# Kernel tuning notes

Hardware: AMD Instinct MI355X
Metric: run time of the kernel (lower is better)

Reference implementation:

```python
import jax, jax.numpy as jnp
import numpy as np

B, T, NN, H = 16, 64, 4096, 1024  # batch, seq_len, num_nodes**2, gru hidden


def _gru_layer(x, w_ih, w_hh, b_ih, b_hh):
    """PyTorch-semantics GRU layer, batch_first. x: [B, T, in] -> [B, T, H]."""
    h_dim = w_hh.shape[1]
    # precompute all input-side gate projections in one GEMM: [B, T, 3H]
    gates_x = jnp.einsum('bti,gi->btg', x, w_ih) + b_ih

    def step(h, gx):
        gh = h @ w_hh.T + b_hh                      # [B, 3H]
        xr, xz, xn = jnp.split(gx, 3, axis=-1)
        hr, hz, hn = jnp.split(gh, 3, axis=-1)
        r = jax.nn.sigmoid(xr + hr)
        z = jax.nn.sigmoid(xz + hz)
        n = jnp.tanh(xn + r * hn)
        h_new = (1.0 - z) * n + z * h
        return h_new, h_new

    h0 = jnp.zeros((x.shape[0], h_dim), x.dtype)
    _, ys = jax.lax.scan(step, h0, jnp.swapaxes(gates_x, 0, 1))  # time-major scan
    return jnp.swapaxes(ys, 0, 1)


def setup_inputs() -> dict:
    key = jax.random.key(0)
    ks = jax.random.split(key, 12)
    s_in, s_h = 1.0 / np.sqrt(NN), 1.0 / np.sqrt(H)
    return {
        'x':       jax.random.normal(ks[0], (B, T, NN), jnp.float32),
        'w_ih_l0': jax.random.normal(ks[1], (3 * H, NN), jnp.float32) * s_in,
        'w_hh_l0': jax.random.normal(ks[2], (3 * H, H), jnp.float32) * s_h,
        'b_ih_l0': jax.random.normal(ks[3], (3 * H,), jnp.float32) * s_h,
        'b_hh_l0': jax.random.normal(ks[4], (3 * H,), jnp.float32) * s_h,
        'w_ih_l1': jax.random.normal(ks[5], (3 * H, H), jnp.float32) * s_h,
        'w_hh_l1': jax.random.normal(ks[6], (3 * H, H), jnp.float32) * s_h,
        'b_ih_l1': jax.random.normal(ks[7], (3 * H,), jnp.float32) * s_h,
        'b_hh_l1': jax.random.normal(ks[8], (3 * H,), jnp.float32) * s_h,
        'dec_w':   jax.random.normal(ks[9], (NN, H), jnp.float32) * s_h,
        'dec_b':   jax.random.normal(ks[10], (NN,), jnp.float32) * s_h,
    }


def reference(x, w_ih_l0, w_hh_l0, b_ih_l0, b_hh_l0,
              w_ih_l1, w_hh_l1, b_ih_l1, b_hh_l1, dec_w, dec_b):
    # 2-layer GRU encode (batch_first), no dropout (eval / drop_p=0)
    h1 = _gru_layer(x, w_ih_l0, w_hh_l0, b_ih_l0, b_hh_l0)
    h2 = _gru_layer(h1, w_ih_l1, w_hh_l1, b_ih_l1, b_hh_l1)
    last = h2[:, -1, :]                               # [B, H] last timestep
    # per-sample decoder loop in the original == one batched GEMM here
    pred_graph_adj = last @ dec_w.T + dec_b           # [B, num_nodes**2]
    return pred_graph_adj
```

## Files before the change

kernel.cpp:

```cpp
#include <hip/hip_runtime.h>
#include <math.h>

constexpr int kB = 16;
constexpr int kT = 64;
constexpr int kH = 1024;

typedef short bf16x8 __attribute__((ext_vector_type(8)));
typedef float floatx4 __attribute__((ext_vector_type(4)));

__device__ __forceinline__ unsigned short f2bf_rne(float f) {
    unsigned u = __float_as_uint(f);
    u = u + 0x7FFFu + ((u >> 16) & 1u);
    return (unsigned short)(u >> 16);
}
__device__ __forceinline__ unsigned f2bf_fast_u(float f) {
    return (__float_as_uint(f) + 0x8000u) >> 16;
}

__device__ __forceinline__ void store_short_sys(unsigned short* p, unsigned v) {
    asm volatile("global_store_short %0, %1, off sc0 sc1"
                 :: "v"(p), "v"(v) : "memory");
}
__device__ __forceinline__ void store_dword_sys(unsigned* p, unsigned v) {
    asm volatile("global_store_dword %0, %1, off sc0 sc1"
                 :: "v"(p), "v"(v) : "memory");
}
__device__ __forceinline__ unsigned load_dword_sys(const unsigned* p) {
    unsigned v;
    asm volatile("global_load_dword %0, %1, off sc0 sc1\n\t"
                 "s_waitcnt vmcnt(0)"
                 : "=v"(v) : "v"(p) : "memory");
    return v;
}

__device__ __forceinline__ void gload_lds16(const unsigned short* g,
                                            unsigned short* lds) {
    __builtin_amdgcn_global_load_lds(
        (const __attribute__((address_space(1))) unsigned int*)(g),
        (__attribute__((address_space(3))) unsigned int*)(lds), 16, 0, 0);
}

__global__ __launch_bounds__(256)
void pack_bf16(const float* __restrict__ src, unsigned short* __restrict__ dst,
               int n4)
{
    const int i = blockIdx.x * 256 + threadIdx.x;
    if (i < n4) {
        const float4 v = ((const float4*)src)[i];
        ushort4 o;
        o.x = f2bf_rne(v.x); o.y = f2bf_rne(v.y);
        o.z = f2bf_rne(v.z); o.w = f2bf_rne(v.w);
        ((ushort4*)dst)[i] = o;
    }
}

#define GBM 64
#define GBN 64
#define GBK 16
#define GPAD 4

__global__ __launch_bounds__(256)
void gemm_nt_bias(const float* __restrict__ X, const float* __restrict__ W,
                  const float* __restrict__ bias, float* __restrict__ C,
                  int M, int N, int K)
{
    __shared__ float Xs[GBK][GBM + GPAD];
    __shared__ float Ws[GBK][GBN + GPAD];

    const int tid = threadIdx.x;
    const int bm = blockIdx.y * GBM;
    const int bn = blockIdx.x * GBN;
    const int tm = (tid >> 4) * 4;
    const int tn = (tid & 15) * 4;
    const int lr = tid >> 2;
    const int lc = (tid & 3) * 4;

    float acc[4][4] = {};

    for (int k0 = 0; k0 < K; k0 += GBK) {
        {
            const int gr = bm + lr;
            float4 v = make_float4(0.f, 0.f, 0.f, 0.f);
            if (gr < M) v = *(const float4*)(X + (long)gr * K + k0 + lc);
            Xs[lc + 0][lr] = v.x; Xs[lc + 1][lr] = v.y;
            Xs[lc + 2][lr] = v.z; Xs[lc + 3][lr] = v.w;
        }
        {
            const int gr = bn + lr;
            const float4 v = *(const float4*)(W + (long)gr * K + k0 + lc);
            Ws[lc + 0][lr] = v.x; Ws[lc + 1][lr] = v.y;
            Ws[lc + 2][lr] = v.z; Ws[lc + 3][lr] = v.w;
        }
        __syncthreads();
        #pragma unroll
        for (int k = 0; k < GBK; ++k) {
            const float4 a4 = *(const float4*)&Xs[k][tm];
            const float4 b4 = *(const float4*)&Ws[k][tn];
            acc[0][0] += a4.x * b4.x; acc[0][1] += a4.x * b4.y; acc[0][2] += a4.x * b4.z; acc[0][3] += a4.x * b4.w;
            acc[1][0] += a4.y * b4.x; acc[1][1] += a4.y * b4.y; acc[1][2] += a4.y * b4.z; acc[1][3] += a4.y * b4.w;
            acc[2][0] += a4.z * b4.x; acc[2][1] += a4.z * b4.y; acc[2][2] += a4.z * b4.z; acc[2][3] += a4.z * b4.w;
            acc[3][0] += a4.w * b4.x; acc[3][1] += a4.w * b4.y; acc[3][2] += a4.w * b4.z; acc[3][3] += a4.w * b4.w;
        }
        __syncthreads();
    }

    #pragma unroll
    for (int i = 0; i < 4; ++i) {
        const int gr = bm + tm + i;
        if (gr >= M) continue;
        #pragma unroll
        for (int jj = 0; jj < 4; ++jj) {
            const int gc = bn + tn + jj;
            C[(long)gr * N + gc] = acc[i][jj] + bias[gc];
        }
    }
}

__global__ __launch_bounds__(256)
void gemm_bf16_a(const unsigned short* __restrict__ X,
                 const unsigned short* __restrict__ W,
                 const float* __restrict__ bias,
                 float* __restrict__ C,
                 int M, int N, int K)
{
    __shared__ __attribute__((aligned(16))) unsigned short As[128 * 32];
    __shared__ __attribute__((aligned(16))) unsigned short Bs[128 * 32];

    const int tid  = threadIdx.x;
    const int lane = tid & 63;
    const int w    = tid >> 6;
    const int wm   = w & 1;
    const int wn   = w >> 1;
    const int bm   = blockIdx.y * 128;
    const int bn   = blockIdx.x * 128;
    const int al   = lane & 15;
    const int aq   = lane >> 4;

    const int srow = lane >> 2;
    const int scol = (lane & 3) * 8;

    floatx4 acc[4][4];
    #pragma unroll
    for (int i = 0; i < 4; ++i)
        #pragma unroll
        for (int j = 0; j < 4; ++j)
            acc[i][j] = (floatx4){0.f, 0.f, 0.f, 0.f};

    for (int k0 = 0; k0 < K; k0 += 32) {
        #pragma unroll
        for (int i = 0; i < 2; ++i) {
            const int r = (w * 2 + i) * 16 + srow;
            gload_lds16(X + (size_t)(bm + r) * K + k0 + scol,
                        As + (w * 2 + i) * 512);
            gload_lds16(W + (size_t)(bn + r) * K + k0 + scol,
                        Bs + (w * 2 + i) * 512);
        }
        __syncthreads();

        bf16x8 af[4], bf[4];
        #pragma unroll
        for (int i = 0; i < 4; ++i)
            af[i] = *(const bf16x8*)&As[(wm * 64 + i * 16 + al) * 32 + aq * 8];
        #pragma unroll
        for (int j = 0; j < 4; ++j)
            bf[j] = *(const bf16x8*)&Bs[(wn * 64 + j * 16 + al) * 32 + aq * 8];
        #pragma unroll
        for (int i = 0; i < 4; ++i)
            #pragma unroll
            for (int j = 0; j < 4; ++j)
                acc[i][j] = __builtin_amdgcn_mfma_f32_16x16x32_bf16(
                    af[i], bf[j], acc[i][j], 0, 0, 0);
        __syncthreads();
    }

    #pragma unroll
    for (int i = 0; i < 4; ++i) {
        #pragma unroll
        for (int j = 0; j < 4; ++j) {
            const int row0 = bm + wm * 64 + i * 16 + aq * 4;
            const int col  = bn + wn * 64 + j * 16 + al;
            const float bv = bias[col];
            #pragma unroll
            for (int r = 0; r < 4; ++r)
                C[(long)(row0 + r) * N + col] = acc[i][j][r] + bv;
        }
    }
}

#define FLAG_STRIDE 4

__global__ __launch_bounds__(768, 3)
void fused_gru_persistent(const float* __restrict__ gx0,
                          const unsigned short* __restrict__ w0, const float* __restrict__ bb0,
                          const unsigned short* __restrict__ w1, const float* __restrict__ bb1,
                          const unsigned short* __restrict__ w2, const float* __restrict__ bb2,
                          unsigned short* __restrict__ h1bf0, unsigned short* __restrict__ h1bf1,
                          unsigned short* __restrict__ h2bf0, unsigned short* __restrict__ h2bf1,
                          float* __restrict__ h2last, unsigned* __restrict__ flags)
{
    __shared__ __attribute__((aligned(16))) floatx4 part[12][3][64];

    const int tid   = threadIdx.x;
    const int lane  = tid & 63;
    const int wid   = tid >> 6;
    const int bx    = blockIdx.x;
    const int jbase = bx * 16;

    const int m  = wid >> 2;
    const int kh = wid & 3;
    const int al = lane & 15;
    const int aq = lane >> 4;

    const unsigned short* Wm = (m == 0) ? w0 : (m == 1) ? w1 : w2;
    const long wbase = (long)(jbase + al) * kH + kh * 256 + aq * 8;
    bf16x8 wreg[3][8];
    #pragma unroll
    for (int g = 0; g < 3; ++g)
        #pragma unroll
        for (int s = 0; s < 8; ++s)
            wreg[g][s] = *(const bf16x8*)(Wm + (long)g * kH * kH + wbase + s * 32);

    const int ub  = tid >> 4;
    const int ujj = tid & 15;
    const int ujg = jbase + ujj;
    const float b0r = bb0[ujg], b0z = bb0[kH + ujg], b0n = bb0[2 * kH + ujg];
    const float b1r = bb1[ujg], b1z = bb1[kH + ujg], b1n = bb1[2 * kH + ujg];
    const float b2r = bb2[ujg], b2z = bb2[kH + ujg], b2n = bb2[2 * kH + ujg];

    float h1reg = 0.f;
    float h2reg = 0.f;

    const int aoff = al * kH + kh * 256 + aq * 8;
    const int pl   = (ub >> 2) * 16 + ujj;
    const int pr   = ub & 3;

    float gxr = 0.f, gxz = 0.f, gxn = 0.f;
    if (tid < 256) {
        const float* g = gx0 + (long)ub * (kT * 3 * kH);
        gxr = g[ujg]; gxz = g[kH + ujg]; gxn = g[2 * kH + ujg];
    }

    for (int k = 0; k <= kT; ++k) {
        const unsigned short* h1p = (k & 1) ? h1bf0 : h1bf1;
        unsigned short*       h1o = (k & 1) ? h1bf1 : h1bf0;
        const unsigned short* h2p = (k & 1) ? h2bf1 : h2bf0;
        unsigned short*       h2o = (k & 1) ? h2bf0 : h2bf1;

        const bool azero = (m < 2) ? (k == 0) : (k <= 1);
        const unsigned short* hsrc = (m < 2) ? h1p : h2p;
        bf16x8 a[8];
        if (!azero) {
            #pragma unroll
            for (int s = 0; s < 8; ++s)
                asm volatile("global_load_dwordx4 %0, %1, off sc0 sc1"
                             : "=&v"(a[s]) : "v"(hsrc + aoff + s * 32) : "memory");
            asm volatile("s_waitcnt vmcnt(0)" ::: "memory");
            __builtin_amdgcn_sched_barrier(0);
        } else {
            #pragma unroll
            for (int s = 0; s < 8; ++s)
                a[s] = (bf16x8){0, 0, 0, 0, 0, 0, 0, 0};
        }

        floatx4 acc[3];
        #pragma unroll
        for (int g = 0; g < 3; ++g) acc[g] = (floatx4){0.f, 0.f, 0.f, 0.f};
        #pragma unroll
        for (int s = 0; s < 8; ++s)
            #pragma unroll
            for (int g = 0; g < 3; ++g)
                acc[g] = __builtin_amdgcn_mfma_f32_16x16x32_bf16(
                    a[s], wreg[g][s], acc[g], 0, 0, 0);

        #pragma unroll
        for (int g = 0; g < 3; ++g)
            part[wid][g][lane] = acc[g];
        __syncthreads();

        if (tid < 256) {
            float gh[3][3];
            #pragma unroll
            for (int mm = 0; mm < 3; ++mm)
                #pragma unroll
                for (int g = 0; g < 3; ++g)
                    gh[mm][g] = part[mm * 4 + 0][g][pl][pr] + part[mm * 4 + 1][g][pl][pr]
                              + part[mm * 4 + 2][g][pl][pr] + part[mm * 4 + 3][g][pl][pr];

            if (k < kT) {
                const float hr = gh[0][0] + b0r;
                const float hz = gh[0][1] + b0z;
                const float hn = gh[0][2] + b0n;
                const float r = 1.f / (1.f + __expf(-(gxr + hr)));
                const float z = 1.f / (1.f + __expf(-(gxz + hz)));
                const float n = tanhf(gxn + r * hn);
                const float hnew = (1.f - z) * n + z * h1reg;
                h1reg = hnew;
                store_short_sys(h1o + ub * kH + ujg, f2bf_fast_u(hnew));
            }
            if (k > 0) {
                const float xr = gh[1][0] + b1r;
                const float xz = gh[1][1] + b1z;
                const float xn = gh[1][2] + b1n;
                const float hr = gh[2][0] + b2r;
                const float hz = gh[2][1] + b2z;
                const float hn = gh[2][2] + b2n;
                const float r = 1.f / (1.f + __expf(-(xr + hr)));
                const float z = 1.f / (1.f + __expf(-(xz + hz)));
                const float n = tanhf(xn + r * hn);
                const float hnew = (1.f - z) * n + z * h2reg;
                h2reg = hnew;
                store_short_sys(h2o + ub * kH + ujg, f2bf_fast_u(hnew));
                if (k == kT) h2last[(long)ub * kH + ujg] = hnew;
            }
        }

        float nxr = 0.f, nxz = 0.f, nxn = 0.f;
        if (tid < 256 && (k + 1) < kT) {
            const float* g = gx0 + (long)ub * (kT * 3 * kH) + (long)(k + 1) * 3 * kH;
            nxr = g[ujg]; nxz = g[kH + ujg]; nxn = g[2 * kH + ujg];
        }

        if (k < kT) {
            __syncthreads();
            if (wid == 0) {
                const unsigned gen = (unsigned)(k + 1);
                if (lane == 0)
                    store_dword_sys(&flags[bx * FLAG_STRIDE], gen);
                while (load_dword_sys(&flags[lane * FLAG_STRIDE]) < gen) {}
            }
            __syncthreads();
        }

        gxr = nxr; gxz = nxz; gxn = nxn;
    }
}

extern "C" void kernel_launch(void* const* d_in, const int* in_sizes, int n_in,
                              void* d_out, int out_size, void* d_ws, size_t ws_size,
                              hipStream_t stream)
{
    const float* x        = (const float*)d_in[0];
    const float* w_ih_l0  = (const float*)d_in[1];
    const float* w_hh_l0  = (const float*)d_in[2];
    const float* b_ih_l0  = (const float*)d_in[3];
    const float* b_hh_l0  = (const float*)d_in[4];
    const float* w_ih_l1  = (const float*)d_in[5];
    const float* w_hh_l1  = (const float*)d_in[6];
    const float* b_ih_l1  = (const float*)d_in[7];
    const float* b_hh_l1  = (const float*)d_in[8];
    const float* dec_w    = (const float*)d_in[9];
    const float* dec_b    = (const float*)d_in[10];
    float* out = (float*)d_out;

    float* ws    = (float*)d_ws;
    float* gx0   = ws;
    unsigned short* h1bf0 = (unsigned short*)(gx0 + (size_t)1024 * 3072);
    unsigned short* h1bf1 = h1bf0 + (size_t)kB * kH;
    unsigned short* h2bf0 = h1bf1 + (size_t)kB * kH;
    unsigned short* h2bf1 = h2bf0 + (size_t)kB * kH;
    float* h2last = (float*)(h2bf1 + (size_t)kB * kH);
    unsigned short* wbf0 = (unsigned short*)(h2last + (size_t)kB * kH);
    unsigned short* wbf1 = wbf0 + (size_t)3 * kH * kH;
    unsigned short* wbf2 = wbf1 + (size_t)3 * kH * kH;
    unsigned short* xbf  = wbf2 + (size_t)3 * kH * kH;
    unsigned short* wihbf = xbf + (size_t)1024 * 4096;
    unsigned* flags = (unsigned*)(wihbf + (size_t)3072 * 4096);

    (void)hipMemsetAsync(flags, 0, 4096, stream);

    const int wn4 = 3 * kH * kH / 4;
    const int xn4 = 1024 * 4096 / 4;
    const int win4 = 3072 * 4096 / 4;

    pack_bf16<<<(wn4 + 255) / 256, 256, 0, stream>>>(w_hh_l0, wbf0, wn4);
    pack_bf16<<<(wn4 + 255) / 256, 256, 0, stream>>>(w_ih_l1, wbf1, wn4);
    pack_bf16<<<(wn4 + 255) / 256, 256, 0, stream>>>(w_hh_l1, wbf2, wn4);
    pack_bf16<<<(xn4 + 255) / 256, 256, 0, stream>>>(x, xbf, xn4);
    pack_bf16<<<(win4 + 255) / 256, 256, 0, stream>>>(w_ih_l0, wihbf, win4);

    gemm_bf16_a<<<dim3(3072 / 128, 1024 / 128), 256, 0, stream>>>(
        xbf, wihbf, b_ih_l0, gx0, 1024, 3072, 4096);

    fused_gru_persistent<<<64, 768, 0, stream>>>(
        gx0, wbf0, b_hh_l0, wbf1, b_ih_l1, wbf2, b_hh_l1,
        h1bf0, h1bf1, h2bf0, h2bf1, h2last, flags);

    gemm_nt_bias<<<dim3(4096 / GBN, 1), 256, 0, stream>>>(
        h2last, dec_w, dec_b, out, kB, 4096, 1024);
}
```

Before: 670.4 us.

## Pipeline input-projection GEMM with 4-stage LDS ring, smaller M tile, and block swizzle

Rewrites the layer-0 input-projection GEMM to use a 4-buffer LDS ring with loads issued two k-steps ahead, synchronized by vmcnt waits and raw barriers. The M tile shrinks from 128 to 64, doubling the grid to 384 blocks, and block IDs are swizzled so neighbouring blocks share operand tiles in cache. The aim is to hide global-to-LDS latency and improve occupancy across CUs. The cost is more LDS per block and hand-tuned wait counts that must stay in step with the number of loads issued per stage.

```diff
diff --git a/kernel.cpp b/kernel.cpp
--- a/kernel.cpp
+++ b/kernel.cpp
@@ -123,61 +123,79 @@
                  float* __restrict__ C,
                  int M, int N, int K)
 {
-    __shared__ __attribute__((aligned(16))) unsigned short As[128 * 32];
-    __shared__ __attribute__((aligned(16))) unsigned short Bs[128 * 32];
+    __shared__ __attribute__((aligned(16))) unsigned short As[4][64 * 32];
+    __shared__ __attribute__((aligned(16))) unsigned short Bs[4][128 * 32];
 
     const int tid  = threadIdx.x;
     const int lane = tid & 63;
     const int w    = tid >> 6;
     const int wm   = w & 1;
     const int wn   = w >> 1;
-    const int bm   = blockIdx.y * 128;
-    const int bn   = blockIdx.x * 128;
     const int al   = lane & 15;
     const int aq   = lane >> 4;
 
+    const int bid = blockIdx.x;
+    const int swz = (bid & 7) * 48 + (bid >> 3);
+    const int bn  = (swz % 24) * 128;
+    const int bm  = (swz / 24) * 64;
+
     const int srow = lane >> 2;
     const int scol = (lane & 3) * 8;
 
-    floatx4 acc[4][4];
+    const int nT = K / 32;
+
+    #define ISSUE_A(buf, k0c)                                                  \
+        gload_lds16(X + (size_t)(bm + w * 16 + srow) * K + (k0c) + scol,       \
+                    &As[buf][(w * 16) * 32]);                                  \
+        gload_lds16(W + (size_t)(bn + w * 32 + srow) * K + (k0c) + scol,       \
+                    &Bs[buf][(w * 32) * 32]);                                  \
+        gload_lds16(W + (size_t)(bn + w * 32 + 16 + srow) * K + (k0c) + scol,  \
+                    &Bs[buf][(w * 32 + 16) * 32]);
+
+    floatx4 acc[2][4];
     #pragma unroll
-    for (int i = 0; i < 4; ++i)
+    for (int i = 0; i < 2; ++i)
         #pragma unroll
         for (int j = 0; j < 4; ++j)
             acc[i][j] = (floatx4){0.f, 0.f, 0.f, 0.f};
 
-    for (int k0 = 0; k0 < K; k0 += 32) {
-        #pragma unroll
-        for (int i = 0; i < 2; ++i) {
-            const int r = (w * 2 + i) * 16 + srow;
-            gload_lds16(X + (size_t)(bm + r) * K + k0 + scol,
-                        As + (w * 2 + i) * 512);
-            gload_lds16(W + (size_t)(bn + r) * K + k0 + scol,
-                        Bs + (w * 2 + i) * 512);
-        }
-        __syncthreads();
-
-        bf16x8 af[4], bf[4];
-        #pragma unroll
-        for (int i = 0; i < 4; ++i)
-            af[i] = *(const bf16x8*)&As[(wm * 64 + i * 16 + al) * 32 + aq * 8];
+    ISSUE_A(0, 0);
+    ISSUE_A(1, 32);
+
+    for (int t = 0; t < nT; ++t) {
+        const int k2 = (t + 2 < nT) ? (t + 2) * 32 : t * 32;
+        const int b2 = (t + 2) & 3;
+        ISSUE_A(b2, k2);
+
+        asm volatile("s_waitcnt vmcnt(6)" ::: "memory");
+        __builtin_amdgcn_s_barrier();
+        asm volatile("" ::: "memory");
+
+        const int cb = t & 3;
+        bf16x8 af[2], bf[4];
+        #pragma unroll
+        for (int i = 0; i < 2; ++i)
+            af[i] = *(const bf16x8*)&As[cb][(wm * 32 + i * 16 + al) * 32 + aq * 8];
         #pragma unroll
         for (int j = 0; j < 4; ++j)
-            bf[j] = *(const bf16x8*)&Bs[(wn * 64 + j * 16 + al) * 32 + aq * 8];
-        #pragma unroll
-        for (int i = 0; i < 4; ++i)
+            bf[j] = *(const bf16x8*)&Bs[cb][(wn * 64 + j * 16 + al) * 32 + aq * 8];
+        #pragma unroll
+        for (int i = 0; i < 2; ++i)
             #pragma unroll
             for (int j = 0; j < 4; ++j)
                 acc[i][j] = __builtin_amdgcn_mfma_f32_16x16x32_bf16(
                     af[i], bf[j], acc[i][j], 0, 0, 0);
-        __syncthreads();
-    }
+
+        asm volatile("" ::: "memory");
+        __builtin_amdgcn_s_barrier();
+    }
+    #undef ISSUE_A
 
     #pragma unroll
-    for (int i = 0; i < 4; ++i) {
+    for (int i = 0; i < 2; ++i) {
         #pragma unroll
         for (int j = 0; j < 4; ++j) {
-            const int row0 = bm + wm * 64 + i * 16 + aq * 4;
+            const int row0 = bm + wm * 32 + i * 16 + aq * 4;
             const int col  = bn + wn * 64 + j * 16 + al;
             const float bv = bias[col];
             #pragma unroll
@@ -378,7 +396,7 @@
     pack_bf16<<<(xn4 + 255) / 256, 256, 0, stream>>>(x, xbf, xn4);
     pack_bf16<<<(win4 + 255) / 256, 256, 0, stream>>>(w_ih_l0, wihbf, win4);
 
-    gemm_bf16_a<<<dim3(3072 / 128, 1024 / 128), 256, 0, stream>>>(
+    gemm_bf16_a<<<384, 256, 0, stream>>>(
         xbf, wihbf, b_ih_l0, gx0, 1024, 3072, 4096);
 
     fused_gru_persistent<<<64, 768, 0, stream>>>(
```

Measured after the change: 666.4 us. Within noise of the previous version (-0.6%).
